# Performance work log

Measured on AMD Instinct MI355X. Metric: run time of the kernel, lower is better.

## Reference

```python
import jax, jax.numpy as jnp
import numpy as np
from jax import lax

D_MODEL = 512
KERNEL = 17
DILATION = 1
MLP_MULT = 4
EPS = 1e-6


def rmsnorm(x, w):
    # x: [B,T,C]; RMSNorm: x * rsqrt(mean(x^2) + eps) * w
    ms = jnp.mean(x * x, axis=-1, keepdims=True)
    return x * lax.rsqrt(ms + EPS) * w


def causal_dwconv(x, w, dilation):
    # x: [B,T,C], w: [C,K]. Equivalent math to the FFT path in the torch code:
    # y[b,t,c] = sum_k w[c,k] * x[b, t - dilation*(K-1) + dilation*k, c] (zeros off left edge)
    B, T, C = x.shape
    K = w.shape[1]
    left_pad = dilation * (K - 1)
    lhs = jnp.transpose(x, (0, 2, 1))          # [B,C,T]
    rhs = w[:, None, :]                        # [C,1,K] depthwise
    y = lax.conv_general_dilated(
        lhs, rhs,
        window_strides=(1,),
        padding=[(left_pad, 0)],
        rhs_dilation=(dilation,),
        dimension_numbers=('NCH', 'OIH', 'NCH'),
        feature_group_count=C,
    )                                          # [B,C,T]
    return jnp.transpose(y, (0, 2, 1))


def setup_inputs() -> dict:
    key = jax.random.key(0)
    ks = jax.random.split(key, 8)
    B, T, d = 4, 16384, D_MODEL
    h = MLP_MULT * d
    scale = lambda fan_in: 1.0 / np.sqrt(fan_in)
    return {
        'x': jax.random.normal(ks[0], (B, T, d), jnp.float32),
        'ln1_w': jnp.ones((d,), jnp.float32),
        'gate_w': jax.random.normal(ks[1], (d, d), jnp.float32) * scale(d),
        'conv_w': jax.random.uniform(ks[2], (d, KERNEL), jnp.float32,
                                     -scale(KERNEL), scale(KERNEL)),
        'proj_w': jax.random.normal(ks[3], (d, d), jnp.float32) * scale(d),
        'ln2_w': jnp.ones((d,), jnp.float32),
        'mlp_w1': jax.random.normal(ks[4], (d, h), jnp.float32) * scale(d),
        'mlp_w2': jax.random.normal(ks[5], (h, d), jnp.float32) * scale(h),
    }


def reference(x, ln1_w, gate_w, conv_w, proj_w, ln2_w, mlp_w1, mlp_w2):
    # Gated depthwise causal conv branch
    hn = rmsnorm(x, ln1_w)
    g = jax.nn.sigmoid(jnp.einsum('btd,de->bte', hn, gate_w))
    hc = causal_dwconv(hn, conv_w, DILATION)
    x = x + jnp.einsum('btd,de->bte', g * hc, proj_w)
    # MLP branch
    hn2 = rmsnorm(x, ln2_w)
    mid = jax.nn.gelu(jnp.einsum('btd,dh->bth', hn2, mlp_w1))
    x = x + jnp.einsum('bth,hd->btd', mid, mlp_w2)
    return x
```

## Files before the change

### kernel.cpp

```cpp
#include <hip/hip_runtime.h>
#include <hip/hip_bf16.h>
#include <cstdint>
#include <cstddef>

typedef __attribute__((ext_vector_type(8))) short short8;
typedef __attribute__((ext_vector_type(4))) short short4v;
typedef __attribute__((ext_vector_type(4))) float floatx4;

#define D_MODEL 512
#define HDIM    2048
#define TSEQ    16384
#define NTOK    65536

__device__ __forceinline__ float bf2f(short s) {
  union { unsigned u; float f; } v; v.u = ((unsigned)(unsigned short)s) << 16; return v.f;
}
__device__ __forceinline__ short f2bf(float f) {
  union { float fv; unsigned u; } v; v.fv = f;
  unsigned u = v.u;
  u += 0x7FFFu + ((u >> 16) & 1u);
  return (short)(u >> 16);
}
__device__ __forceinline__ void gload_lds16(const void* g, void* l) {
  __builtin_amdgcn_global_load_lds((const __attribute__((address_space(1))) void*)g,
                                   (__attribute__((address_space(3))) void*)l, 16, 0, 0);
}

__global__ void wt_transpose(const float* __restrict__ W, short* __restrict__ Wt,
                             const int K, const int N) {
  __shared__ float t[64][65];
  const int tid = threadIdx.x;
  const long k0 = (long)blockIdx.x * 64;
  const long n0 = (long)blockIdx.y * 64;
  const int rr = tid >> 4;
  const int cc = (tid & 15) * 4;
#pragma unroll
  for (int i = 0; i < 4; ++i) {
    const int r = rr + i * 16;
    const float4 v = *(const float4*)(W + (k0 + r) * N + n0 + cc);
    t[r][cc + 0] = v.x; t[r][cc + 1] = v.y; t[r][cc + 2] = v.z; t[r][cc + 3] = v.w;
  }
  __syncthreads();
#pragma unroll
  for (int i = 0; i < 4; ++i) {
    const int n = rr + i * 16;
    short4v o;
    o[0] = f2bf(t[cc + 0][n]);
    o[1] = f2bf(t[cc + 1][n]);
    o[2] = f2bf(t[cc + 2][n]);
    o[3] = f2bf(t[cc + 3][n]);
    *(short4v*)(Wt + (n0 + n) * K + k0 + cc) = o;
  }
}

__global__ void convw_transpose(const float* __restrict__ cw, float* __restrict__ wT) {
  const int idx = blockIdx.x * 256 + threadIdx.x;
  if (idx >= 17 * D_MODEL) return;
  const int k = idx / D_MODEL;
  const int c = idx % D_MODEL;
  wT[idx] = cw[c * 17 + k];
}

__global__ void rmsnorm_kernel(const float* __restrict__ x, const float* __restrict__ w,
                               short* __restrict__ outp) {
  const int lane = threadIdx.x & 63;
  const long row = (long)blockIdx.x * 4 + (threadIdx.x >> 6);
  const float* xr = x + row * D_MODEL + lane * 8;
  const float4 a = *(const float4*)xr;
  const float4 b = *(const float4*)(xr + 4);
  float ss = a.x * a.x + a.y * a.y + a.z * a.z + a.w * a.w
           + b.x * b.x + b.y * b.y + b.z * b.z + b.w * b.w;
#pragma unroll
  for (int m = 32; m; m >>= 1) ss += __shfl_xor(ss, m);
  const float scale = rsqrtf(ss * (1.0f / D_MODEL) + 1e-6f);
  const float4 wa = *(const float4*)(w + lane * 8);
  const float4 wb = *(const float4*)(w + lane * 8 + 4);
  short8 o;
  o[0] = f2bf(a.x * scale * wa.x);
  o[1] = f2bf(a.y * scale * wa.y);
  o[2] = f2bf(a.z * scale * wa.z);
  o[3] = f2bf(a.w * scale * wa.w);
  o[4] = f2bf(b.x * scale * wb.x);
  o[5] = f2bf(b.y * scale * wb.y);
  o[6] = f2bf(b.z * scale * wb.z);
  o[7] = f2bf(b.w * scale * wb.w);
  *(short8*)(outp + row * D_MODEL + lane * 8) = o;
}

__global__ void dwconv_kernel(const short* __restrict__ hn, const float* __restrict__ wT,
                              short* __restrict__ hc) {
  const int tid = threadIdx.x;
  const int chunk = tid & 63;
  const long row = (long)blockIdx.x * 4 + (tid >> 6);
  const int t = (int)(row & (TSEQ - 1));
  const int c0 = chunk * 8;
  float acc[8];
#pragma unroll
  for (int j = 0; j < 8; ++j) acc[j] = 0.f;
  const int kmin = (t >= 16) ? 0 : (16 - t);
  for (int k = kmin; k < 17; ++k) {
    const short8 h = *(const short8*)(hn + (row - 16 + k) * D_MODEL + c0);
    const float* wp = wT + k * D_MODEL + c0;
    const float4 w0 = *(const float4*)(wp);
    const float4 w1 = *(const float4*)(wp + 4);
    acc[0] += bf2f(h[0]) * w0.x;
    acc[1] += bf2f(h[1]) * w0.y;
    acc[2] += bf2f(h[2]) * w0.z;
    acc[3] += bf2f(h[3]) * w0.w;
    acc[4] += bf2f(h[4]) * w1.x;
    acc[5] += bf2f(h[5]) * w1.y;
    acc[6] += bf2f(h[6]) * w1.z;
    acc[7] += bf2f(h[7]) * w1.w;
  }
  short8 o;
#pragma unroll
  for (int j = 0; j < 8; ++j) o[j] = f2bf(acc[j]);
  *(short8*)(hc + row * D_MODEL + c0) = o;
}

#define PHASE_BAR() __builtin_amdgcn_s_barrier()
#define LGKM0() { asm volatile("s_waitcnt lgkmcnt(0)" ::: "memory"); __builtin_amdgcn_sched_barrier(0); }
#define VMC8()  { asm volatile("s_waitcnt vmcnt(8)"   ::: "memory"); __builtin_amdgcn_sched_barrier(0); }
#define VMC0()  { asm volatile("s_waitcnt vmcnt(0)"   ::: "memory"); __builtin_amdgcn_sched_barrier(0); }
#define DSR1(dst, addr, imm) \
  asm volatile("ds_read_b128 %0, %1 offset:%2" : "=v"(dst) : "v"(addr), "i"(imm))

template <int EPI>
__global__ __launch_bounds__(256, 2)
void gemm128(const short* __restrict__ A, const short* __restrict__ Bt,
             const int K, const int N, const int nbn,
             const void* __restrict__ aux, void* __restrict__ outp) {
  __shared__ short Alds[2 * 128 * 64];
  __shared__ short Blds[2 * 128 * 64];
  const int tid = threadIdx.x;
  const int lane = tid & 63;
  const int w = tid >> 6;
  const int wm = w >> 1;
  const int wn = w & 1;

  const int nwg = gridDim.x;
  const int cpx = nwg >> 3;
  const int bid = blockIdx.x;
  const int wid = (bid & 7) * cpx + (bid >> 3);
  const int brow = (wid / nbn) * 128;
  const int bcol = (wid % nbn) * 128;

  floatx4 acc[4][4];
#pragma unroll
  for (int i = 0; i < 4; ++i)
#pragma unroll
    for (int j = 0; j < 4; ++j) acc[i][j] = {0.f, 0.f, 0.f, 0.f};

  short8 af[4][2];
  short8 bfr[4][2];

  const int chunkx = (lane & 7) ^ (lane >> 3);
  const short* gA = A + ((long)(brow + w * 32 + (lane >> 3))) * K + chunkx * 8;
  const short* gB = Bt + ((long)(bcol + w * 32 + (lane >> 3))) * K + chunkx * 8;
  const int kchunk = lane >> 4;

  const unsigned Abase = (unsigned)(uintptr_t)(__attribute__((address_space(3))) short*)Alds;
  const unsigned Bbase = (unsigned)(uintptr_t)(__attribute__((address_space(3))) short*)Blds;
  const unsigned lanelo = (unsigned)((lane & 15) * 128);
  const unsigned c0t = (unsigned)(((0 + kchunk) ^ (lane & 7)) * 16);
  const unsigned c1t = (unsigned)(((4 + kchunk) ^ (lane & 7)) * 16);
  const unsigned adrA0 = Abase + (unsigned)(wm * 8192) + lanelo + c0t;
  const unsigned adrA1 = Abase + (unsigned)(wm * 8192) + lanelo + c1t;
  const unsigned adrB0 = Bbase + (unsigned)(wn * 8192) + lanelo + c0t;
  const unsigned adrB1 = Bbase + (unsigned)(wn * 8192) + lanelo + c1t;

#define STG(BUF, koff)                                                         \
  { _Pragma("unroll")                                                          \
    for (int j = 0; j < 4; ++j)                                                \
      gload_lds16(gA + (long)j * 8 * K + (koff),                               \
                  &Alds[((BUF) * 128 + w * 32 + j * 8) * 64]);                 \
    _Pragma("unroll")                                                          \
    for (int j = 0; j < 4; ++j)                                                \
      gload_lds16(gB + (long)j * 8 * K + (koff),                               \
                  &Blds[((BUF) * 128 + w * 32 + j * 8) * 64]); }

#define READS(BUF) {                                                           \
    DSR1(af[0][0],  adrA0, (BUF)*16384 + 0*2048);                              \
    DSR1(af[0][1],  adrA1, (BUF)*16384 + 0*2048);                              \
    DSR1(af[1][0],  adrA0, (BUF)*16384 + 1*2048);                              \
    DSR1(af[1][1],  adrA1, (BUF)*16384 + 1*2048);                              \
    DSR1(af[2][0],  adrA0, (BUF)*16384 + 2*2048);                              \
    DSR1(af[2][1],  adrA1, (BUF)*16384 + 2*2048);                              \
    DSR1(af[3][0],  adrA0, (BUF)*16384 + 3*2048);                              \
    DSR1(af[3][1],  adrA1, (BUF)*16384 + 3*2048);                              \
    DSR1(bfr[0][0], adrB0, (BUF)*16384 + 0*2048);                              \
    DSR1(bfr[0][1], adrB1, (BUF)*16384 + 0*2048);                              \
    DSR1(bfr[1][0], adrB0, (BUF)*16384 + 1*2048);                              \
    DSR1(bfr[1][1], adrB1, (BUF)*16384 + 1*2048);                              \
    DSR1(bfr[2][0], adrB0, (BUF)*16384 + 2*2048);                              \
    DSR1(bfr[2][1], adrB1, (BUF)*16384 + 2*2048);                              \
    DSR1(bfr[3][0], adrB0, (BUF)*16384 + 3*2048);                              \
    DSR1(bfr[3][1], adrB1, (BUF)*16384 + 3*2048); }

#define MMACL_ALL()                                                            \
  { __builtin_amdgcn_s_setprio(1);                                             \
    _Pragma("unroll")                                                          \
    for (int mi = 0; mi < 4; ++mi)                                             \
      _Pragma("unroll")                                                        \
      for (int ni = 0; ni < 4; ++ni)                                           \
        _Pragma("unroll")                                                      \
        for (int ks = 0; ks < 2; ++ks)                                         \
          acc[mi][ni] = __builtin_amdgcn_mfma_f32_16x16x32_bf16(               \
              af[mi][ks], bfr[ni][ks], acc[mi][ni], 0, 0, 0);                  \
    __builtin_amdgcn_s_setprio(0); }

#define TILE(BUF, DOST, W8, W0, LASTT, koff)                                   \
  {                                                                            \
    if (DOST) STG((BUF) ^ 1, koff);                                            \
    if (W8) VMC8();                                                            \
    if (W0) VMC0();                                                            \
    PHASE_BAR();                                                               \
    READS(BUF); LGKM0();                                                       \
    MMACL_ALL();                                                               \
    if (!LASTT) PHASE_BAR();                                                   \
  }

  STG(0, 0);

  const int nkt = K >> 6;
  for (int kt = 0; kt < nkt - 2; kt += 2) {
    TILE(0, 1, 1, 0, 0, (kt + 1) * 64);
    TILE(1, 1, 1, 0, 0, (kt + 2) * 64);
  }
  TILE(0, 1, 1, 0, 0, (nkt - 1) * 64);
  TILE(1, 0, 0, 1, 1, 0);

#undef TILE
#undef MMACL_ALL
#undef READS
#undef STG

#pragma unroll
  for (int mi = 0; mi < 4; ++mi) {
    const int r0 = brow + wm * 64 + mi * 16 + (lane >> 4) * 4;
#pragma unroll
    for (int j = 0; j < 4; ++j) {
      const int rb = (r0 + j) * N;
      const int gcb = bcol + wn * 64 + (lane & 15);
#pragma unroll
      for (int ni = 0; ni < 4; ++ni) {
        const int idx = rb + gcb + ni * 16;
        const float v = acc[mi][ni][j];
        if (EPI == 0) {
          const float hcv = bf2f(((const short*)aux)[idx]);
          const float g = 1.f / (1.f + __expf(-v));
          ((short*)outp)[idx] = f2bf(g * hcv);
        } else if (EPI == 1) {
          ((float*)outp)[idx] = ((const float*)aux)[idx] + v;
        } else if (EPI == 2) {
          const float x3 = v * v * v;
          const float z = 0.7978845608028654f * (v + 0.044715f * x3);
          const float th = 1.f - 2.f / (__expf(2.f * z) + 1.f);
          ((short*)outp)[idx] = f2bf(0.5f * v * (1.f + th));
        } else {
          ((float*)outp)[idx] += v;
        }
      }
    }
  }
}

extern "C" void kernel_launch(void* const* d_in, const int* in_sizes, int n_in,
                              void* d_out, int out_size, void* d_ws, size_t ws_size,
                              hipStream_t stream) {
  const float* x      = (const float*)d_in[0];
  const float* ln1_w  = (const float*)d_in[1];
  const float* gate_w = (const float*)d_in[2];
  const float* conv_w = (const float*)d_in[3];
  const float* proj_w = (const float*)d_in[4];
  const float* ln2_w  = (const float*)d_in[5];
  const float* mlp_w1 = (const float*)d_in[6];
  const float* mlp_w2 = (const float*)d_in[7];
  float* out = (float*)d_out;
  char* ws = (char*)d_ws;

  short* hn      = (short*)(ws + 0);
  short* hc      = (short*)(ws + 67108864L);
  short* mid     = (short*)(ws + 134217728L);
  short* gate_wt = (short*)(ws + 402653184L);
  short* proj_wt = (short*)(ws + 403177472L);
  short* w1t     = (short*)(ws + 403701760L);
  short* w2t     = (short*)(ws + 405798912L);
  float* convwT  = (float*)(ws + 407896064L);

  const dim3 b256(256);

  wt_transpose<<<dim3(8, 8),  b256, 0, stream>>>(gate_w, gate_wt, 512, 512);
  wt_transpose<<<dim3(8, 8),  b256, 0, stream>>>(proj_w, proj_wt, 512, 512);
  wt_transpose<<<dim3(8, 32), b256, 0, stream>>>(mlp_w1, w1t, 512, 2048);
  wt_transpose<<<dim3(32, 8), b256, 0, stream>>>(mlp_w2, w2t, 2048, 512);
  convw_transpose<<<34, b256, 0, stream>>>(conv_w, convwT);

  rmsnorm_kernel<<<NTOK / 4, b256, 0, stream>>>(x, ln1_w, hn);
  dwconv_kernel<<<NTOK / 4, b256, 0, stream>>>(hn, convwT, hc);
  gemm128<0><<<512 * 4, b256, 0, stream>>>(hn, gate_wt, 512, 512, 4, hc, hc);
  gemm128<1><<<512 * 4, b256, 0, stream>>>(hc, proj_wt, 512, 512, 4, x, out);
  rmsnorm_kernel<<<NTOK / 4, b256, 0, stream>>>(out, ln2_w, hn);
  gemm128<2><<<512 * 16, b256, 0, stream>>>(hn, w1t, 512, 2048, 16, nullptr, mid);
  gemm128<3><<<512 * 4, b256, 0, stream>>>(mid, w2t, 2048, 512, 4, nullptr, out);
}
```

Baseline: 721.2 us.

## Stage GEMM epilogue through LDS for vectorized coalesced global stores

Rewrites the GEMM epilogue so accumulators are first written into a padded LDS tile, then each thread reads 32 contiguous columns and performs vectorized 16-byte loads and stores of the auxiliary inputs and outputs. This replaces scattered scalar 2- or 4-byte global accesses with coalesced wide ones, meant to cut epilogue memory-transaction cost. It merges the A/B LDS buffers into one 64KB region reused for the transpose, which adds two extra barriers. It also drops the s_setprio raise around the MFMA block.

```diff
diff --git a/kernel.cpp b/kernel.cpp
--- a/kernel.cpp
+++ b/kernel.cpp
@@ -130,8 +130,10 @@
 void gemm128(const short* __restrict__ A, const short* __restrict__ Bt,
              const int K, const int N, const int nbn,
              const void* __restrict__ aux, void* __restrict__ outp) {
-  __shared__ short Alds[2 * 128 * 64];
-  __shared__ short Blds[2 * 128 * 64];
+  __shared__ __align__(16) char smem[65536];
+  short* Alds = (short*)smem;
+  short* Blds = (short*)(smem + 32768);
+  float* tbuf = (float*)smem;
   const int tid = threadIdx.x;
   const int lane = tid & 63;
   const int w = tid >> 6;
@@ -159,8 +161,8 @@
   const short* gB = Bt + ((long)(bcol + w * 32 + (lane >> 3))) * K + chunkx * 8;
   const int kchunk = lane >> 4;
 
-  const unsigned Abase = (unsigned)(uintptr_t)(__attribute__((address_space(3))) short*)Alds;
-  const unsigned Bbase = (unsigned)(uintptr_t)(__attribute__((address_space(3))) short*)Blds;
+  const unsigned Abase = (unsigned)(uintptr_t)(__attribute__((address_space(3))) char*)smem;
+  const unsigned Bbase = Abase + 32768u;
   const unsigned lanelo = (unsigned)((lane & 15) * 128);
   const unsigned c0t = (unsigned)(((0 + kchunk) ^ (lane & 7)) * 16);
   const unsigned c1t = (unsigned)(((4 + kchunk) ^ (lane & 7)) * 16);
@@ -198,16 +200,14 @@
     DSR1(bfr[3][1], adrB1, (BUF)*16384 + 3*2048); }
 
 #define MMACL_ALL()                                                            \
-  { __builtin_amdgcn_s_setprio(1);                                             \
-    _Pragma("unroll")                                                          \
+  { _Pragma("unroll")                                                          \
     for (int mi = 0; mi < 4; ++mi)                                             \
       _Pragma("unroll")                                                        \
       for (int ni = 0; ni < 4; ++ni)                                           \
         _Pragma("unroll")                                                      \
         for (int ks = 0; ks < 2; ++ks)                                         \
           acc[mi][ni] = __builtin_amdgcn_mfma_f32_16x16x32_bf16(               \
-              af[mi][ks], bfr[ni][ks], acc[mi][ni], 0, 0, 0);                  \
-    __builtin_amdgcn_s_setprio(0); }
+              af[mi][ks], bfr[ni][ks], acc[mi][ni], 0, 0, 0); }
 
 #define TILE(BUF, DOST, W8, W0, LASTT, koff)                                   \
   {                                                                            \
@@ -235,33 +235,84 @@
 #undef READS
 #undef STG
 
-#pragma unroll
-  for (int mi = 0; mi < 4; ++mi) {
-    const int r0 = brow + wm * 64 + mi * 16 + (lane >> 4) * 4;
-#pragma unroll
-    for (int j = 0; j < 4; ++j) {
-      const int rb = (r0 + j) * N;
-      const int gcb = bcol + wn * 64 + (lane & 15);
-#pragma unroll
-      for (int ni = 0; ni < 4; ++ni) {
-        const int idx = rb + gcb + ni * 16;
-        const float v = acc[mi][ni][j];
-        if (EPI == 0) {
-          const float hcv = bf2f(((const short*)aux)[idx]);
-          const float g = 1.f / (1.f + __expf(-v));
-          ((short*)outp)[idx] = f2bf(g * hcv);
-        } else if (EPI == 1) {
-          ((float*)outp)[idx] = ((const float*)aux)[idx] + v;
-        } else if (EPI == 2) {
-          const float x3 = v * v * v;
-          const float z = 0.7978845608028654f * (v + 0.044715f * x3);
-          const float th = 1.f - 2.f / (__expf(2.f * z) + 1.f);
-          ((short*)outp)[idx] = f2bf(0.5f * v * (1.f + th));
-        } else {
-          ((float*)outp)[idx] += v;
+  __syncthreads();
+  const int rl_rd = tid >> 2;
+  const int cbi   = tid & 3;
+#pragma unroll
+  for (int p = 0; p < 2; ++p) {
+    if (wm == p) {
+#pragma unroll
+      for (int mi = 0; mi < 4; ++mi) {
+        const int rloc = mi * 16 + ((lane >> 4) << 2);
+#pragma unroll
+        for (int ni = 0; ni < 4; ++ni) {
+          const int c = wn * 64 + ni * 16 + (lane & 15);
+          const int base = (c >> 5) * 33 + (c & 31);
+#pragma unroll
+          for (int j = 0; j < 4; ++j)
+            tbuf[(rloc + j) * 132 + base] = acc[mi][ni][j];
         }
       }
     }
+    __syncthreads();
+    {
+      float v[32];
+      const int rb = rl_rd * 132 + cbi * 33;
+#pragma unroll
+      for (int i = 0; i < 32; ++i) v[i] = tbuf[rb + i];
+      const int grow = brow + p * 64 + rl_rd;
+      const int gcol = bcol + cbi * 32;
+      const long gidx = (long)grow * N + gcol;
+      if (EPI == 0) {
+        const short* hcp = (const short*)aux + gidx;
+        short* op = (short*)outp + gidx;
+#pragma unroll
+        for (int q = 0; q < 4; ++q) {
+          const short8 hv = *(const short8*)(hcp + q * 8);
+          short8 o;
+#pragma unroll
+          for (int e = 0; e < 8; ++e) {
+            const float g = 1.f / (1.f + __expf(-v[q * 8 + e]));
+            o[e] = f2bf(g * bf2f(hv[e]));
+          }
+          *(short8*)(op + q * 8) = o;
+        }
+      } else if (EPI == 1) {
+        const float* xp = (const float*)aux + gidx;
+        float* op = (float*)outp + gidx;
+#pragma unroll
+        for (int q = 0; q < 8; ++q) {
+          float4 xv = *(const float4*)(xp + q * 4);
+          xv.x += v[q * 4 + 0]; xv.y += v[q * 4 + 1];
+          xv.z += v[q * 4 + 2]; xv.w += v[q * 4 + 3];
+          *(float4*)(op + q * 4) = xv;
+        }
+      } else if (EPI == 2) {
+        short* op = (short*)outp + gidx;
+#pragma unroll
+        for (int q = 0; q < 4; ++q) {
+          short8 o;
+#pragma unroll
+          for (int e = 0; e < 8; ++e) {
+            const float x = v[q * 8 + e];
+            const float z = 0.7978845608028654f * (x + 0.044715f * x * x * x);
+            const float th = 1.f - 2.f / (__expf(2.f * z) + 1.f);
+            o[e] = f2bf(0.5f * x * (1.f + th));
+          }
+          *(short8*)(op + q * 8) = o;
+        }
+      } else {
+        float* op = (float*)outp + gidx;
+#pragma unroll
+        for (int q = 0; q < 8; ++q) {
+          float4 ov = *(const float4*)(op + q * 4);
+          ov.x += v[q * 4 + 0]; ov.y += v[q * 4 + 1];
+          ov.z += v[q * 4 + 2]; ov.w += v[q * 4 + 3];
+          *(float4*)(op + q * 4) = ov;
+        }
+      }
+    }
+    if (p == 0) __syncthreads();
   }
 }
 
```

Result: slower. 761.4 us (+5.6%).
